# Performance work log

Hardware: AMD Instinct MI355X
Metric: run time of the kernel (lower is better)

The kernel has to match this reference:

```python
import jax, jax.numpy as jnp
import numpy as np

K = 3            # kernel_size
S = 4            # up_factor
VMAX = 1.0
TAU = 0.5
CENTER_BIAS = 2.5
SMOOTH_RES = 0.15
C_IN = 21
HIDDEN = 48
B_, H0, W0 = 4, 81, 81
CTR = K // 2      # = 1, also GL recursion depth M


def _dir_step_diff(k):
    """Precompute (base_pos - base_neg) per direction/step: [8, M+1, k, k]."""
    c = k // 2
    dirs = np.array([[1, 0], [1, 1], [0, 1], [-1, 1], [-1, 0], [-1, -1], [0, -1], [1, -1]], np.float32)
    dirs = dirs / (np.linalg.norm(dirs, axis=1, keepdims=True) + 1e-8)
    yy, xx = np.meshgrid(np.arange(k), np.arange(k), indexing='ij')
    rel = np.stack([yy - c, xx - c], -1).astype(np.float32)
    diff = np.zeros((8, c + 1, k, k), np.float32)
    for d in range(8):
        v = dirs[d]
        proj = rel[..., 0] * v[1] + rel[..., 1] * v[0]
        step = np.clip(np.round(proj), -c, c).astype(np.int64)
        for m in range(c + 1):
            diff[d, m] = (step == m).astype(np.float32) - (step == -m).astype(np.float32)
    return diff

DIFF = jnp.asarray(_dir_step_diff(K))  # [8, M+1, K, K]


def conv3x3(x, w, b):
    y = jax.lax.conv_general_dilated(x, w, (1, 1), 'SAME',
                                     dimension_numbers=('NCHW', 'OIHW', 'NCHW'))
    return y + b[None, :, None, None]


def bilinear_up(x, s):
    """F.interpolate(scale_factor=s, mode='bilinear', align_corners=True)."""
    B, C, h, w = x.shape
    H, W = h * s, w * s
    ys = jnp.linspace(0.0, h - 1.0, H)
    xs = jnp.linspace(0.0, w - 1.0, W)
    y0 = jnp.clip(jnp.floor(ys).astype(jnp.int32), 0, h - 2)
    x0 = jnp.clip(jnp.floor(xs).astype(jnp.int32), 0, w - 2)
    wy = (ys - y0)[:, None]
    wx = (xs - x0)[None, :]
    x00 = x[:, :, y0][:, :, :, x0]
    x01 = x[:, :, y0][:, :, :, x0 + 1]
    x10 = x[:, :, y0 + 1][:, :, :, x0]
    x11 = x[:, :, y0 + 1][:, :, :, x0 + 1]
    return (x00 * (1 - wy) * (1 - wx) + x01 * (1 - wy) * wx
            + x10 * wy * (1 - wx) + x11 * wy * wx)


def setup_inputs() -> dict:
    key = jax.random.key(0)
    ks = jax.random.split(key, 6)
    wn = lambda k, shape: jax.random.normal(k, shape, jnp.float32) * 0.05
    return {
        'x': jax.random.normal(ks[0], (B_, C_IN, H0, W0), jnp.float32),
        'w1o': wn(ks[1], (HIDDEN, C_IN, 3, 3)), 'b1o': jnp.zeros((HIDDEN,), jnp.float32),
        'w2o': wn(ks[2], (8, HIDDEN, 3, 3)), 'b2o': jnp.zeros((8,), jnp.float32),
        'w1g': wn(ks[3], (HIDDEN, C_IN, 3, 3)), 'b1g': jnp.zeros((HIDDEN,), jnp.float32),
        'w2g': wn(ks[4], (1, HIDDEN, 3, 3)), 'b2g': jnp.zeros((1,), jnp.float32),
        'beta': jnp.asarray(1.6, jnp.float32),
    }


def reference(x, w1o, b1o, w2o, b2o, w1g, b1g, w2g, b2g, beta):
    B, C, h, w = x.shape
    c = CTR
    # heads
    raw_v = conv3x3(jax.nn.relu(conv3x3(x, w1o, b1o)), w2o, b2o)          # [B,8,h,w]
    g = jax.nn.sigmoid(conv3x3(jax.nn.relu(conv3x3(x, w1g, b1g)), w2g, b2g))  # [B,1,h,w]
    v = VMAX * jnp.tanh(raw_v)
    # Gruenwald-Letnikov coefficients, M = center (=1 for k=3)
    coeffs = [jnp.ones_like(v)]
    wm = coeffs[0]
    for m in range(1, c + 1):
        wm = wm * (v - m + 1.0) / m * -1.0
        coeffs.append(wm)
    coeff = jnp.stack(coeffs, axis=2)                                      # [B,8,M+1,h,w]
    # direction kernels, averaged over the 8 directions
    ker = jnp.einsum('bdmhw,dmkl->bklhw', coeff, DIFF) / 8.0               # [B,K,K,h,w]
    mask_pre = ker.reshape(B, K * K, h, w)
    ci = c * K + c
    # NOTE: torch adds center_bias in-place on a view of ker -> ker itself is biased too
    mask_pre = mask_pre.at[:, ci].add(CENTER_BIAS)
    ker_b = mask_pre.reshape(B, K, K, h, w)
    mask_lp = jax.nn.softmax(mask_pre / TAU, axis=1)                       # [B,9,h,w]
    # unfold 3x3 window with reflect padding
    xp = jnp.pad(x, ((0, 0), (0, 0), (c, c), (c, c)), mode='reflect')
    patches = jnp.stack([xp[:, :, i:i + h, j:j + w]
                         for i in range(K) for j in range(K)], axis=2)     # [B,C,9,h,w]
    rep2 = lambda a, ax: jnp.repeat(jnp.repeat(a, S, axis=ax), S, axis=ax + 1)
    neigh = rep2(patches, 3)                                               # [B,C,9,H,W]
    mask_lp_u = rep2(mask_lp, 2)                                           # [B,9,H,W]
    g_up = rep2(g, 2)                                                      # [B,1,H,W]
    x_up = bilinear_up(x, S)                                               # [B,C,H,W]
    y_lp_out = jnp.einsum('bcnHW,bnHW->bcHW', neigh, mask_lp_u)
    lam = SMOOTH_RES * (1.0 - g_up)
    y_lp = x_up + lam * (y_lp_out - x_up)
    # highpass branch (mode='both')
    ker_hp = ker_b - ker_b.mean(axis=(1, 2), keepdims=True)
    ker_hp = ker_hp / (jnp.abs(ker_hp).sum(axis=(1, 2), keepdims=True) + 1e-8)
    mask_hp = rep2(ker_hp.reshape(B, K * K, h, w), 2)
    y_hp = jnp.einsum('bcnHW,bnHW->bcHW', neigh, mask_hp)
    y = y_lp + jnp.tanh(beta) * g_up * y_hp
    return (y, v, g_up)
```

## Files before the change

### kernel.cpp

```cpp
#include <hip/hip_runtime.h>
#include <math.h>

#define B_N   4
#define CIN   21
#define HIDC  48
#define H0    81
#define NP    6561
#define HH    324
#define NPH   104976

__device__ __forceinline__ float tanh_fast(float x) {
    float e = __expf(2.f * x);
    return 1.f - 2.f / (e + 1.f);
}

__global__ __launch_bounds__(256) void k1_conv1(
    const float* __restrict__ x,
    const float* __restrict__ w1o, const float* __restrict__ b1o,
    const float* __restrict__ w1g, const float* __restrict__ b1g,
    float* __restrict__ hid_o, float* __restrict__ hid_g)
{
    __shared__ __align__(16) float xs[CIN * 18 * 20];
    __shared__ __align__(16) float wt[189 * 16];
    __shared__ float bs[16];
    const int tid = threadIdx.x;
    const int tile = blockIdx.x, ocg = blockIdx.y, b = blockIdx.z;
    const int ty0 = (tile / 6) * 16, tx0 = (tile % 6) * 16;
    const float* xb = x + (size_t)b * CIN * NP;

    for (int pos = tid; pos < 324; pos += 256) {
        const int yy = pos / 18, xx = pos - yy * 18;
        const int gy = ty0 - 1 + yy, gx = tx0 - 1 + xx;
        const bool ok = ((unsigned)gy < (unsigned)H0) && ((unsigned)gx < (unsigned)H0);
        const int gidx = gy * H0 + gx;
        #pragma unroll 3
        for (int ic = 0; ic < CIN; ic++)
            xs[ic * 360 + yy * 20 + xx] = ok ? xb[ic * NP + gidx] : 0.f;
    }
    for (int i = tid; i < 189 * 16; i += 256) {
        const int ict = i >> 4, oc = i & 15;
        const int oc96 = ocg * 16 + oc;
        wt[i] = (oc96 < 48) ? w1o[oc96 * 189 + ict] : w1g[(oc96 - 48) * 189 + ict];
    }
    if (tid < 16) {
        const int oc96 = ocg * 16 + tid;
        bs[tid] = (oc96 < 48) ? b1o[oc96] : b1g[oc96 - 48];
    }
    __syncthreads();

    const int og = tid >> 6;
    const int q  = tid & 63;
    const int qy = q >> 2, qx4 = (q & 3) * 4;
    const int oc4 = og * 4;

    float acc[4][4];
    #pragma unroll
    for (int i = 0; i < 4; i++)
        #pragma unroll
        for (int j = 0; j < 4; j++) acc[i][j] = bs[oc4 + j];

    for (int ic = 0; ic < CIN; ic++) {
        #pragma unroll
        for (int ky = 0; ky < 3; ky++) {
            const float4 f0 = *(const float4*)&xs[ic * 360 + (qy + ky) * 20 + qx4];
            const float4 f1 = *(const float4*)&xs[ic * 360 + (qy + ky) * 20 + qx4 + 4];
            const float xw[8] = {f0.x, f0.y, f0.z, f0.w, f1.x, f1.y, f1.z, f1.w};
            #pragma unroll
            for (int kx = 0; kx < 3; kx++) {
                const float4 wv = *(const float4*)&wt[(ic * 9 + ky * 3 + kx) * 16 + oc4];
                const float wj[4] = {wv.x, wv.y, wv.z, wv.w};
                #pragma unroll
                for (int i = 0; i < 4; i++)
                    #pragma unroll
                    for (int j = 0; j < 4; j++)
                        acc[i][j] = fmaf(xw[i + kx], wj[j], acc[i][j]);
            }
        }
    }

    const int oy = ty0 + qy;
    if (oy < H0) {
        #pragma unroll
        for (int j = 0; j < 4; j++) {
            const int oc96 = ocg * 16 + oc4 + j;
            float* base = (oc96 < 48)
                ? hid_o + ((size_t)b * HIDC + oc96) * NP
                : hid_g + ((size_t)b * HIDC + (oc96 - 48)) * NP;
            #pragma unroll
            for (int i = 0; i < 4; i++) {
                const int ox = tx0 + qx4 + i;
                if (ox < H0) base[oy * H0 + ox] = fmaxf(acc[i][j], 0.f);
            }
        }
    }
}

__global__ __launch_bounds__(256) void k2_conv2_masks(
    const float* __restrict__ hid_o, const float* __restrict__ hid_g,
    const float* __restrict__ w2o, const float* __restrict__ b2o,
    const float* __restrict__ w2g, const float* __restrict__ b2g,
    float* __restrict__ v_out,
    float* __restrict__ g_buf, float* __restrict__ m_lp, float* __restrict__ m_hp)
{
    __shared__ __align__(16) float wo_s[HIDC * 9 * 8];
    __shared__ float wg_s[HIDC * 9];
    __shared__ float red[4][32][12];
    __shared__ float res_s[32][28];
    const int tid = threadIdx.x;
    const int b = blockIdx.y;

    for (int i = tid; i < HIDC * 9 * 8; i += 256) {
        const int d = i / (HIDC * 9), r = i - d * (HIDC * 9);
        wo_s[r * 8 + d] = w2o[i];
    }
    for (int i = tid; i < HIDC * 9; i += 256) wg_s[i] = w2g[i];
    __syncthreads();

    const int pxl = tid & 31;
    const int s   = tid >> 5;
    const int w   = tid >> 6;
    const int px  = blockIdx.x * 32 + pxl;
    const bool valid = (px < NP);
    const int oy = px / H0, ox = px - oy * H0;
    const int ic0 = s * 6;
    const float* po = hid_o + ((size_t)b * HIDC + ic0) * NP;
    const float* pg = hid_g + ((size_t)b * HIDC + ic0) * NP;

    float a[8] = {0.f, 0.f, 0.f, 0.f, 0.f, 0.f, 0.f, 0.f};
    float ag = 0.f;

    #pragma unroll 1
    for (int ky = 0; ky < 3; ky++) {
        const int iy = oy + ky - 1;
        const bool rok = valid && ((unsigned)iy < (unsigned)H0);
        #pragma unroll
        for (int kx = 0; kx < 3; kx++) {
            const int ix = ox + kx - 1;
            const bool ok = rok && ((unsigned)ix < (unsigned)H0);
            const int off = iy * H0 + ix;
            const int tap = ky * 3 + kx;
            #pragma unroll
            for (int j = 0; j < 6; j++) {
                const float vo = ok ? po[j * NP + off] : 0.f;
                const float vg = ok ? pg[j * NP + off] : 0.f;
                const int wb = ((ic0 + j) * 9 + tap) * 8;
                const float4 wA = *(const float4*)&wo_s[wb];
                const float4 wB = *(const float4*)&wo_s[wb + 4];
                a[0] = fmaf(vo, wA.x, a[0]); a[1] = fmaf(vo, wA.y, a[1]);
                a[2] = fmaf(vo, wA.z, a[2]); a[3] = fmaf(vo, wA.w, a[3]);
                a[4] = fmaf(vo, wB.x, a[4]); a[5] = fmaf(vo, wB.y, a[5]);
                a[6] = fmaf(vo, wB.z, a[6]); a[7] = fmaf(vo, wB.w, a[7]);
                ag = fmaf(vg, wg_s[(ic0 + j) * 9 + tap], ag);
            }
        }
    }

    #pragma unroll
    for (int n = 0; n < 8; n++) a[n] += __shfl_xor(a[n], 32);
    ag += __shfl_xor(ag, 32);
    if ((tid & 32) == 0) {
        #pragma unroll
        for (int n = 0; n < 8; n++) red[w][pxl][n] = a[n];
        red[w][pxl][8] = ag;
    }
    __syncthreads();

    if (tid < 32 && valid) {
        float v[8];
        #pragma unroll
        for (int n = 0; n < 8; n++)
            v[n] = tanh_fast(red[0][tid][n] + red[1][tid][n] + red[2][tid][n]
                             + red[3][tid][n] + b2o[n]);
        const float agf = red[0][tid][8] + red[1][tid][8] + red[2][tid][8]
                        + red[3][tid][8] + b2g[0];
        const float g = 1.f / (1.f + __expf(-agf));

        constexpr float DT[8][9] = {
            {-1, 0, 1, -1, 0, 1, -1, 0, 1},
            {-1,-1, 0, -1, 0, 1,  0, 1, 1},
            {-1,-1,-1,  0, 0, 0,  1, 1, 1},
            { 0,-1,-1,  1, 0,-1,  1, 1, 0},
            { 1, 0,-1,  1, 0,-1,  1, 0,-1},
            { 1, 1, 0,  1, 0,-1,  0,-1,-1},
            { 1, 1, 1,  0, 0, 0, -1,-1,-1},
            { 0, 1, 1, -1, 0, 1, -1,-1, 0}};
        float ker[9];
        #pragma unroll
        for (int n = 0; n < 9; n++) {
            float t = 0.f;
            #pragma unroll
            for (int d = 0; d < 8; d++) t += v[d] * DT[d][n];
            ker[n] = -0.125f * t;
        }
        ker[4] += 2.5f;
        float mx = ker[0];
        #pragma unroll
        for (int n = 1; n < 9; n++) mx = fmaxf(mx, ker[n]);
        float exn[9], sum = 0.f;
        #pragma unroll
        for (int n = 0; n < 9; n++) { exn[n] = __expf((ker[n] - mx) * 2.0f); sum += exn[n]; }
        const float rs = 1.f / sum;
        float mean = 0.f;
        #pragma unroll
        for (int n = 0; n < 9; n++) mean += ker[n];
        mean *= (1.f / 9.f);
        float den = 1e-8f;
        #pragma unroll
        for (int n = 0; n < 9; n++) den += fabsf(ker[n] - mean);
        const float rd = 1.f / den;

        #pragma unroll
        for (int n = 0; n < 8; n++) res_s[tid][n] = v[n];
        res_s[tid][8] = g;
        #pragma unroll
        for (int n = 0; n < 9; n++) {
            res_s[tid][9 + n]  = exn[n] * rs;
            res_s[tid][18 + n] = (ker[n] - mean) * rd;
        }
    }
    __syncthreads();

    const int px0 = blockIdx.x * 32;
    for (int j = tid; j < 27 * 32; j += 256) {
        const int plane = j >> 5, pl = j & 31;
        const int p = px0 + pl;
        if (p >= NP) continue;
        const float val = res_s[pl][plane];
        float* dst;
        if (plane < 8)        dst = v_out + ((size_t)b * 8 + plane) * NP;
        else if (plane == 8)  dst = g_buf + (size_t)b * NP;
        else if (plane < 18)  dst = m_lp + ((size_t)b * 9 + (plane - 9)) * NP;
        else                  dst = m_hp + ((size_t)b * 9 + (plane - 18)) * NP;
        dst[p] = val;
    }
}

__global__ __launch_bounds__(256) void k3_agg(
    const float* __restrict__ x, const float* __restrict__ m_lp,
    const float* __restrict__ m_hp,
    float* __restrict__ a_lp, float* __restrict__ a_hp)
{
    const int pix = blockIdx.x * 256 + threadIdx.x;
    if (pix >= NP) return;
    const int c = blockIdx.y, b = blockIdx.z;
    const int oy = pix / H0, ox = pix - oy * H0;
    float ml[9], mh[9];
    const float* mlb = m_lp + (size_t)b * 9 * NP + pix;
    const float* mhb = m_hp + (size_t)b * 9 * NP + pix;
    #pragma unroll
    for (int n = 0; n < 9; n++) { ml[n] = mlb[n * NP]; mh[n] = mhb[n * NP]; }
    const float* xc = x + ((size_t)b * CIN + c) * NP;
    float alp = 0.f, ahp = 0.f;
    #pragma unroll
    for (int ky = 0; ky < 3; ky++) {
        int iy = oy + ky - 1;
        iy = iy < 0 ? -iy : (iy > H0 - 1 ? 2 * (H0 - 1) - iy : iy);
        #pragma unroll
        for (int kx = 0; kx < 3; kx++) {
            int ix = ox + kx - 1;
            ix = ix < 0 ? -ix : (ix > H0 - 1 ? 2 * (H0 - 1) - ix : ix);
            const float p = xc[iy * H0 + ix];
            const int n = ky * 3 + kx;
            alp = fmaf(p, ml[n], alp);
            ahp = fmaf(p, mh[n], ahp);
        }
    }
    a_lp[((size_t)b * CIN + c) * NP + pix] = alp;
    a_hp[((size_t)b * CIN + c) * NP + pix] = ahp;
}

__global__ __launch_bounds__(256) void k4_up(
    const float* __restrict__ x, const float* __restrict__ g_buf,
    const float* __restrict__ a_lp, const float* __restrict__ a_hp,
    const float* __restrict__ beta,
    float* __restrict__ y_out, float* __restrict__ gup_out)
{
    const int tid = threadIdx.x;
    if (tid >= 243) return;
    const int c = blockIdx.y;
    const int b = blockIdx.z;
    const int H = blockIdx.x * 3 + tid / 81;
    const int wq = tid % 81;
    const int h0r = H >> 2;
    const float g = g_buf[(size_t)b * NP + h0r * H0 + wq];
    if (c == CIN) {
        *reinterpret_cast<float4*>(gup_out + (size_t)b * NPH + H * HH + wq * 4) =
            make_float4(g, g, g, g);
        return;
    }
    const float tb = tanh_fast(beta[0]);
    const float alp = a_lp[((size_t)b * CIN + c) * NP + h0r * H0 + wq];
    const float ahp = a_hp[((size_t)b * CIN + c) * NP + h0r * H0 + wq];
    const float lam = 0.15f * (1.f - g);
    const float gh = tb * g;
    const float* xc = x + ((size_t)b * CIN + c) * NP;
    const float ysf = (float)H * (80.f / 323.f);
    int y0 = (int)ysf;
    if (y0 > H0 - 2) y0 = H0 - 2;
    const float wy = ysf - (float)y0;
    const float* r0 = xc + y0 * H0;
    const float* r1 = r0 + H0;
    float res[4];
    #pragma unroll
    for (int i = 0; i < 4; i++) {
        const int W = wq * 4 + i;
        const float xsf = (float)W * (80.f / 323.f);
        int x0 = (int)xsf;
        if (x0 > H0 - 2) x0 = H0 - 2;
        const float wx = xsf - (float)x0;
        const float x00 = r0[x0], x01 = r0[x0 + 1];
        const float x10 = r1[x0], x11 = r1[x0 + 1];
        const float top = x00 + (x01 - x00) * wx;
        const float bot = x10 + (x11 - x10) * wx;
        const float xup = top + (bot - top) * wy;
        res[i] = xup + lam * (alp - xup) + gh * ahp;
    }
    *reinterpret_cast<float4*>(y_out + ((size_t)b * CIN + c) * NPH + H * HH + wq * 4) =
        make_float4(res[0], res[1], res[2], res[3]);
}

extern "C" void kernel_launch(void* const* d_in, const int* in_sizes, int n_in,
                              void* d_out, int out_size, void* d_ws, size_t ws_size,
                              hipStream_t stream)
{
    const float* x    = (const float*)d_in[0];
    const float* w1o  = (const float*)d_in[1];
    const float* b1o  = (const float*)d_in[2];
    const float* w2o  = (const float*)d_in[3];
    const float* b2o  = (const float*)d_in[4];
    const float* w1g  = (const float*)d_in[5];
    const float* b1g  = (const float*)d_in[6];
    const float* w2g  = (const float*)d_in[7];
    const float* b2g  = (const float*)d_in[8];
    const float* beta = (const float*)d_in[9];
    float* out = (float*)d_out;
    float* wsf = (float*)d_ws;

    float* hid_o = wsf;
    float* hid_g = hid_o + (size_t)B_N * HIDC * NP;
    float* m_lp  = hid_g + (size_t)B_N * HIDC * NP;
    float* m_hp  = m_lp + (size_t)B_N * 9 * NP;
    float* g_buf = m_hp + (size_t)B_N * 9 * NP;
    float* a_lp  = g_buf + (size_t)B_N * NP;
    float* a_hp  = a_lp + (size_t)B_N * CIN * NP;

    float* y_out = out;
    float* v_out = out + (size_t)B_N * CIN * NPH;
    float* gup   = v_out + (size_t)B_N * 8 * NP;

    k1_conv1<<<dim3(36, 6, B_N), 256, 0, stream>>>(x, w1o, b1o, w1g, b1g, hid_o, hid_g);
    k2_conv2_masks<<<dim3((NP + 31) / 32, B_N), 256, 0, stream>>>(
        hid_o, hid_g, w2o, b2o, w2g, b2g, v_out, g_buf, m_lp, m_hp);
    k3_agg<<<dim3((NP + 255) / 256, CIN, B_N), 256, 0, stream>>>(x, m_lp, m_hp, a_lp, a_hp);
    k4_up<<<dim3(108, CIN + 1, B_N), 256, 0, stream>>>(x, g_buf, a_lp, a_hp, beta, y_out, gup);
}
```

Measured before the change: 171.9 us.

## Fuse mask aggregation into upsample kernel and widen conv1 output-channel tile

```diff
diff --git a/kernel.cpp b/kernel.cpp
--- a/kernel.cpp
+++ b/kernel.cpp
@@ -21,8 +21,8 @@
     float* __restrict__ hid_o, float* __restrict__ hid_g)
 {
     __shared__ __align__(16) float xs[CIN * 18 * 20];
-    __shared__ __align__(16) float wt[189 * 16];
-    __shared__ float bs[16];
+    __shared__ __align__(16) float wt[189 * 32];
+    __shared__ float bs[32];
     const int tid = threadIdx.x;
     const int tile = blockIdx.x, ocg = blockIdx.y, b = blockIdx.z;
     const int ty0 = (tile / 6) * 16, tx0 = (tile % 6) * 16;
@@ -37,13 +37,13 @@
         for (int ic = 0; ic < CIN; ic++)
             xs[ic * 360 + yy * 20 + xx] = ok ? xb[ic * NP + gidx] : 0.f;
     }
-    for (int i = tid; i < 189 * 16; i += 256) {
-        const int ict = i >> 4, oc = i & 15;
-        const int oc96 = ocg * 16 + oc;
+    for (int i = tid; i < 189 * 32; i += 256) {
+        const int ict = i >> 5, oc = i & 31;
+        const int oc96 = ocg * 32 + oc;
         wt[i] = (oc96 < 48) ? w1o[oc96 * 189 + ict] : w1g[(oc96 - 48) * 189 + ict];
     }
-    if (tid < 16) {
-        const int oc96 = ocg * 16 + tid;
+    if (tid < 32) {
+        const int oc96 = ocg * 32 + tid;
         bs[tid] = (oc96 < 48) ? b1o[oc96] : b1g[oc96 - 48];
     }
     __syncthreads();
@@ -51,13 +51,13 @@
     const int og = tid >> 6;
     const int q  = tid & 63;
     const int qy = q >> 2, qx4 = (q & 3) * 4;
-    const int oc4 = og * 4;
-
-    float acc[4][4];
+    const int oc8 = og * 8;
+
+    float acc[4][8];
     #pragma unroll
     for (int i = 0; i < 4; i++)
         #pragma unroll
-        for (int j = 0; j < 4; j++) acc[i][j] = bs[oc4 + j];
+        for (int j = 0; j < 8; j++) acc[i][j] = bs[oc8 + j];
 
     for (int ic = 0; ic < CIN; ic++) {
         #pragma unroll
@@ -67,29 +67,35 @@
             const float xw[8] = {f0.x, f0.y, f0.z, f0.w, f1.x, f1.y, f1.z, f1.w};
             #pragma unroll
             for (int kx = 0; kx < 3; kx++) {
-                const float4 wv = *(const float4*)&wt[(ic * 9 + ky * 3 + kx) * 16 + oc4];
-                const float wj[4] = {wv.x, wv.y, wv.z, wv.w};
+                const float4 wa = *(const float4*)&wt[(ic * 9 + ky * 3 + kx) * 32 + oc8];
+                const float4 wb = *(const float4*)&wt[(ic * 9 + ky * 3 + kx) * 32 + oc8 + 4];
+                const float wj[8] = {wa.x, wa.y, wa.z, wa.w, wb.x, wb.y, wb.z, wb.w};
                 #pragma unroll
                 for (int i = 0; i < 4; i++)
                     #pragma unroll
-                    for (int j = 0; j < 4; j++)
+                    for (int j = 0; j < 8; j++)
                         acc[i][j] = fmaf(xw[i + kx], wj[j], acc[i][j]);
             }
         }
     }
 
     const int oy = ty0 + qy;
+    const int ox0 = tx0 + qx4;
     if (oy < H0) {
         #pragma unroll
-        for (int j = 0; j < 4; j++) {
-            const int oc96 = ocg * 16 + oc4 + j;
+        for (int j = 0; j < 8; j++) {
+            const int oc96 = ocg * 32 + oc8 + j;
             float* base = (oc96 < 48)
                 ? hid_o + ((size_t)b * HIDC + oc96) * NP
                 : hid_g + ((size_t)b * HIDC + (oc96 - 48)) * NP;
-            #pragma unroll
-            for (int i = 0; i < 4; i++) {
-                const int ox = tx0 + qx4 + i;
-                if (ox < H0) base[oy * H0 + ox] = fmaxf(acc[i][j], 0.f);
+            if (ox0 + 3 < H0) {
+                *reinterpret_cast<float4*>(base + oy * H0 + ox0) =
+                    make_float4(fmaxf(acc[0][j], 0.f), fmaxf(acc[1][j], 0.f),
+                                fmaxf(acc[2][j], 0.f), fmaxf(acc[3][j], 0.f));
+            } else {
+                #pragma unroll
+                for (int i = 0; i < 4; i++)
+                    if (ox0 + i < H0) base[oy * H0 + ox0 + i] = fmaxf(acc[i][j], 0.f);
             }
         }
     }
@@ -235,43 +241,9 @@
     }
 }
 
-__global__ __launch_bounds__(256) void k3_agg(
-    const float* __restrict__ x, const float* __restrict__ m_lp,
-    const float* __restrict__ m_hp,
-    float* __restrict__ a_lp, float* __restrict__ a_hp)
-{
-    const int pix = blockIdx.x * 256 + threadIdx.x;
-    if (pix >= NP) return;
-    const int c = blockIdx.y, b = blockIdx.z;
-    const int oy = pix / H0, ox = pix - oy * H0;
-    float ml[9], mh[9];
-    const float* mlb = m_lp + (size_t)b * 9 * NP + pix;
-    const float* mhb = m_hp + (size_t)b * 9 * NP + pix;
-    #pragma unroll
-    for (int n = 0; n < 9; n++) { ml[n] = mlb[n * NP]; mh[n] = mhb[n * NP]; }
-    const float* xc = x + ((size_t)b * CIN + c) * NP;
-    float alp = 0.f, ahp = 0.f;
-    #pragma unroll
-    for (int ky = 0; ky < 3; ky++) {
-        int iy = oy + ky - 1;
-        iy = iy < 0 ? -iy : (iy > H0 - 1 ? 2 * (H0 - 1) - iy : iy);
-        #pragma unroll
-        for (int kx = 0; kx < 3; kx++) {
-            int ix = ox + kx - 1;
-            ix = ix < 0 ? -ix : (ix > H0 - 1 ? 2 * (H0 - 1) - ix : ix);
-            const float p = xc[iy * H0 + ix];
-            const int n = ky * 3 + kx;
-            alp = fmaf(p, ml[n], alp);
-            ahp = fmaf(p, mh[n], ahp);
-        }
-    }
-    a_lp[((size_t)b * CIN + c) * NP + pix] = alp;
-    a_hp[((size_t)b * CIN + c) * NP + pix] = ahp;
-}
-
 __global__ __launch_bounds__(256) void k4_up(
     const float* __restrict__ x, const float* __restrict__ g_buf,
-    const float* __restrict__ a_lp, const float* __restrict__ a_hp,
+    const float* __restrict__ m_lp, const float* __restrict__ m_hp,
     const float* __restrict__ beta,
     float* __restrict__ y_out, float* __restrict__ gup_out)
 {
@@ -282,24 +254,47 @@
     const int H = blockIdx.x * 3 + tid / 81;
     const int wq = tid % 81;
     const int h0r = H >> 2;
-    const float g = g_buf[(size_t)b * NP + h0r * H0 + wq];
+    const int lpx = h0r * H0 + wq;
+    const float g = g_buf[(size_t)b * NP + lpx];
     if (c == CIN) {
         *reinterpret_cast<float4*>(gup_out + (size_t)b * NPH + H * HH + wq * 4) =
             make_float4(g, g, g, g);
         return;
     }
+    float ml[9], mh[9];
+    const float* mlb = m_lp + (size_t)b * 9 * NP + lpx;
+    const float* mhb = m_hp + (size_t)b * 9 * NP + lpx;
+    #pragma unroll
+    for (int n = 0; n < 9; n++) { ml[n] = mlb[n * NP]; mh[n] = mhb[n * NP]; }
+    const float* xc = x + ((size_t)b * CIN + c) * NP;
+    float p[3][3];
+    #pragma unroll
+    for (int ky = 0; ky < 3; ky++) {
+        int iy = h0r + ky - 1;
+        iy = iy < 0 ? -iy : (iy > H0 - 1 ? 2 * (H0 - 1) - iy : iy);
+        #pragma unroll
+        for (int kx = 0; kx < 3; kx++) {
+            int ix = wq + kx - 1;
+            ix = ix < 0 ? -ix : (ix > H0 - 1 ? 2 * (H0 - 1) - ix : ix);
+            p[ky][kx] = xc[iy * H0 + ix];
+        }
+    }
+    float alp = 0.f, ahp = 0.f;
+    #pragma unroll
+    for (int ky = 0; ky < 3; ky++)
+        #pragma unroll
+        for (int kx = 0; kx < 3; kx++) {
+            alp = fmaf(p[ky][kx], ml[ky * 3 + kx], alp);
+            ahp = fmaf(p[ky][kx], mh[ky * 3 + kx], ahp);
+        }
     const float tb = tanh_fast(beta[0]);
-    const float alp = a_lp[((size_t)b * CIN + c) * NP + h0r * H0 + wq];
-    const float ahp = a_hp[((size_t)b * CIN + c) * NP + h0r * H0 + wq];
     const float lam = 0.15f * (1.f - g);
     const float gh = tb * g;
-    const float* xc = x + ((size_t)b * CIN + c) * NP;
     const float ysf = (float)H * (80.f / 323.f);
     int y0 = (int)ysf;
     if (y0 > H0 - 2) y0 = H0 - 2;
     const float wy = ysf - (float)y0;
-    const float* r0 = xc + y0 * H0;
-    const float* r1 = r0 + H0;
+    const int sy = y0 - h0r + 1;
     float res[4];
     #pragma unroll
     for (int i = 0; i < 4; i++) {
@@ -308,8 +303,11 @@
         int x0 = (int)xsf;
         if (x0 > H0 - 2) x0 = H0 - 2;
         const float wx = xsf - (float)x0;
-        const float x00 = r0[x0], x01 = r0[x0 + 1];
-        const float x10 = r1[x0], x11 = r1[x0 + 1];
+        const int sx = x0 - wq + 1;
+        const float x00 = sy == 0 ? (sx == 0 ? p[0][0] : p[0][1]) : (sx == 0 ? p[1][0] : p[1][1]);
+        const float x01 = sy == 0 ? (sx == 0 ? p[0][1] : p[0][2]) : (sx == 0 ? p[1][1] : p[1][2]);
+        const float x10 = sy == 0 ? (sx == 0 ? p[1][0] : p[1][1]) : (sx == 0 ? p[2][0] : p[2][1]);
+        const float x11 = sy == 0 ? (sx == 0 ? p[1][1] : p[1][2]) : (sx == 0 ? p[2][1] : p[2][2]);
         const float top = x00 + (x01 - x00) * wx;
         const float bot = x10 + (x11 - x10) * wx;
         const float xup = top + (bot - top) * wy;
@@ -341,16 +339,13 @@
     float* m_lp  = hid_g + (size_t)B_N * HIDC * NP;
     float* m_hp  = m_lp + (size_t)B_N * 9 * NP;
     float* g_buf = m_hp + (size_t)B_N * 9 * NP;
-    float* a_lp  = g_buf + (size_t)B_N * NP;
-    float* a_hp  = a_lp + (size_t)B_N * CIN * NP;
 
     float* y_out = out;
     float* v_out = out + (size_t)B_N * CIN * NPH;
     float* gup   = v_out + (size_t)B_N * 8 * NP;
 
-    k1_conv1<<<dim3(36, 6, B_N), 256, 0, stream>>>(x, w1o, b1o, w1g, b1g, hid_o, hid_g);
+    k1_conv1<<<dim3(36, 3, B_N), 256, 0, stream>>>(x, w1o, b1o, w1g, b1g, hid_o, hid_g);
     k2_conv2_masks<<<dim3((NP + 31) / 32, B_N), 256, 0, stream>>>(
         hid_o, hid_g, w2o, b2o, w2g, b2g, v_out, g_buf, m_lp, m_hp);
-    k3_agg<<<dim3((NP + 255) / 256, CIN, B_N), 256, 0, stream>>>(x, m_lp, m_hp, a_lp, a_hp);
-    k4_up<<<dim3(108, CIN + 1, B_N), 256, 0, stream>>>(x, g_buf, a_lp, a_hp, beta, y_out, gup);
-}
+    k4_up<<<dim3(108, CIN + 1, B_N), 256, 0, stream>>>(x, g_buf, m_lp, m_hp, beta, y_out, gup);
+}
```

Result: faster. 153.8 us (-10.5%).
